# Optimization experiments

Hardware: AMD Instinct MI355X
Metric: run time of the kernel (lower is better)

Reference implementation:

```python
import jax, jax.numpy as jnp
import numpy as np

BN_EPS = 1e-5
K = 3  # kernel size


def conv2d(x, w, b, pad):
    y = jax.lax.conv_general_dilated(
        x, w, window_strides=(1, 1), padding=[(pad, pad), (pad, pad)],
        dimension_numbers=('NCHW', 'OIHW', 'NCHW'))
    return y + b[None, :, None, None]


def setup_inputs() -> dict:
    key = jax.random.key(0)
    ks = jax.random.split(key, 4)
    B, C, H, W, O = 8, 256, 64, 64, 256
    x = jax.random.normal(ks[0], (B, C, H, W), dtype=jnp.float32)
    # offset/mask conv: 3*dg*k*k = 27 out channels; small init -> small offsets
    w_off = jax.random.normal(ks[1], (27, C, K, K), dtype=jnp.float32) * 0.01
    b_off = jnp.zeros((27,), dtype=jnp.float32)
    # main deformable conv weight/bias
    w = jax.random.normal(ks[2], (O, C, K, K), dtype=jnp.float32) * 0.05
    b = jnp.zeros((O,), dtype=jnp.float32)
    # BatchNorm (inference) params / running stats
    gamma = jnp.ones((O,), dtype=jnp.float32)
    beta = jnp.zeros((O,), dtype=jnp.float32)
    run_mean = jnp.zeros((O,), dtype=jnp.float32)
    run_var = jnp.ones((O,), dtype=jnp.float32)
    return {"x": x, "w_off": w_off, "b_off": b_off, "w": w, "b": b,
            "gamma": gamma, "beta": beta, "run_mean": run_mean, "run_var": run_var}


def _dcn_bn_relu(x, w_off, b_off, w, b, gamma, beta, run_mean, run_var):
    B, C, H, W = x.shape
    KK = K * K
    # offset + modulation mask (DCNv2): channels [0:9]=dy, [9:18]=dx, [18:27]=mask
    om = conv2d(x, w_off, b_off, pad=1)            # [B, 27, H, W]
    dy, dx = om[:, :KK], om[:, KK:2 * KK]          # [B, 9, H, W]
    mod = jax.nn.sigmoid(om[:, 2 * KK:])           # [B, 9, H, W]

    ky, kx = jnp.meshgrid(jnp.arange(K), jnp.arange(K), indexing='ij')
    # base sampling grid: out pixel + dilation*(k - center), padding=1
    base_y = jnp.arange(H, dtype=jnp.float32)[None, :, None] - 1.0 + ky.reshape(KK, 1, 1)
    base_x = jnp.arange(W, dtype=jnp.float32)[None, None, :] - 1.0 + kx.reshape(KK, 1, 1)
    py = base_y[None] + dy                          # [B, 9, H, W]
    px = base_x[None] + dx

    y0 = jnp.floor(py); x0 = jnp.floor(px)
    fy = py - y0; fx = px - x0
    y0 = y0.astype(jnp.int32); x0 = x0.astype(jnp.int32)

    x_flat = x.reshape(B, C, H * W)
    gather = jax.vmap(lambda xf, idx: xf[:, idx])   # ([C,HW],[9,H,W]) -> [C,9,H,W]

    def corner(yi, xi, wgt):
        valid = (yi >= 0) & (yi < H) & (xi >= 0) & (xi < W)
        idx = jnp.clip(yi, 0, H - 1) * W + jnp.clip(xi, 0, W - 1)
        val = gather(x_flat, idx)                   # [B, C, 9, H, W]
        return val * (wgt * valid.astype(wgt.dtype))[:, None]

    sampled = (corner(y0,     x0,     (1 - fy) * (1 - fx))
               + corner(y0,     x0 + 1, (1 - fy) * fx)
               + corner(y0 + 1, x0,     fy * (1 - fx))
               + corner(y0 + 1, x0 + 1, fy * fx))    # [B, C, 9, H, W]
    sampled = sampled * mod[:, None]                 # modulation

    O = w.shape[0]
    out = jnp.einsum('bckhw,ock->bohw', sampled, w.reshape(O, C, KK))
    out = out + b[None, :, None, None]

    # BatchNorm2d (inference) + ReLU
    inv = gamma / jnp.sqrt(run_var + BN_EPS)
    out = out * inv[None, :, None, None] + (beta - run_mean * inv)[None, :, None, None]
    return jax.nn.relu(out)


def reference(x, w_off, b_off, w, b, gamma, beta, run_mean, run_var):
    return _dcn_bn_relu(x, w_off, b_off, w, b, gamma, beta, run_mean, run_var)
```

## Files before the change

### kernel.cpp

```cpp
#include <hip/hip_runtime.h>
#include <math.h>

#define B_   8
#define C_   256
#define H_   64
#define W_   64
#define O_   256
#define KK_  9
#define CK_  2304
#define HW_  4096
#define BN_EPS 1e-5f

typedef __bf16 bf16x8 __attribute__((ext_vector_type(8)));
typedef float  f32x4  __attribute__((ext_vector_type(4)));

static __device__ __forceinline__ unsigned short f2bf(float f) {
    unsigned int u = __float_as_uint(f);
    unsigned int r = (u + 0x7fffu + ((u >> 16) & 1u)) >> 16;
    return (unsigned short)r;
}
static __device__ __forceinline__ unsigned int packbf2(float lo, float hi) {
    unsigned int ul = __float_as_uint(lo) + 0x8000u;
    unsigned int uh = __float_as_uint(hi) + 0x8000u;
    return __builtin_amdgcn_perm(uh, ul, 0x07060302u);
}
static __device__ __forceinline__ float bflo(unsigned int u) {
    return __uint_as_float(u << 16);
}
static __device__ __forceinline__ float bfhi(unsigned int u) {
    return __uint_as_float(u & 0xffff0000u);
}

__global__ __launch_bounds__(256) void prep_kernel(
    const float* __restrict__ x, const float* __restrict__ w,
    const float* __restrict__ w_off,
    unsigned short* __restrict__ xT, unsigned short* __restrict__ wKf,
    unsigned short* __restrict__ wof)
{
    __shared__ float tile[64][65];
    __shared__ float wbuf[4608];

    const int blk = blockIdx.x;
    const int tid = threadIdx.x, lane = tid & 63, tg = tid >> 6;

    if (blk < 512) {
        const int b = blk & 7, h = blk >> 3;
        const int hwb = h * W_;
#pragma unroll
        for (int ct = 0; ct < 4; ++ct) {
            const int c0 = ct * 64;
#pragma unroll
            for (int r = 0; r < 16; ++r) {
                int c_l = tg + r * 4;
                tile[c_l][lane] = x[((size_t)(b * C_ + c0 + c_l)) * HW_ + hwb + lane];
            }
            __syncthreads();
#pragma unroll
            for (int it = 0; it < 4; ++it) {
                const int hw_l = tg * 16 + it * 4 + (lane >> 4);
                const int c_l4 = (lane & 15) * 4;
                float v0 = tile[c_l4 + 0][hw_l];
                float v1 = tile[c_l4 + 1][hw_l];
                float v2 = tile[c_l4 + 2][hw_l];
                float v3 = tile[c_l4 + 3][hw_l];
                uint2 pk;
                pk.x = packbf2(v0, v1);
                pk.y = packbf2(v2, v3);
                *(uint2*)&xT[((size_t)(b * HW_ + hwb + hw_l)) * C_ + c0 + c_l4] = pk;
            }
            __syncthreads();
        }
    } else if (blk < 640) {
        const int t2 = blk - 512;
        const int NT = t2 >> 3, cb = t2 & 7;
#pragma unroll
        for (int i = 0; i < 18; ++i) {
            int j = i * 256 + tid;
            int o_l = j / 288, rest = j - o_l * 288;
            wbuf[o_l * 288 + rest] = w[(size_t)(NT * 16 + o_l) * CK_ + cb * 288 + rest];
        }
        __syncthreads();
#pragma unroll
        for (int i = 0; i < 18; ++i) {
            int d = i * 256 + tid;
            int tap = d >> 9, r5 = d & 511;
            int ln = r5 >> 3, e = r5 & 7;
            int n16 = ln & 15, q = ln >> 4;
            float val = wbuf[n16 * 288 + (q * 8 + e) * 9 + tap];
            wKf[((size_t)(NT * 72 + tap * 8 + cb) * 64 + ln) * 8 + e] = f2bf(val);
        }
    } else {
        const int t2 = blk - 640;
        const int NT = t2 >> 3, cb = t2 & 7;
#pragma unroll
        for (int i = 0; i < 18; ++i) {
            int j = i * 256 + tid;
            int o_l = j / 288, rest = j - o_l * 288;
            int o = NT * 16 + o_l;
            wbuf[o_l * 288 + rest] =
                (o < 27) ? w_off[(size_t)o * CK_ + cb * 288 + rest] : 0.f;
        }
        __syncthreads();
#pragma unroll
        for (int i = 0; i < 18; ++i) {
            int d = i * 256 + tid;
            int tap = d >> 9, r5 = d & 511;
            int ln = r5 >> 3, e = r5 & 7;
            int n16 = ln & 15, q = ln >> 4;
            float val = wbuf[n16 * 288 + (q * 8 + e) * 9 + tap];
            wof[((size_t)(NT * 72 + tap * 8 + cb) * 64 + ln) * 8 + e] = f2bf(val);
        }
    }
}

__global__ __launch_bounds__(512, 4) void dcn_fused_kernel(
    const unsigned short* __restrict__ xT, const unsigned short* __restrict__ wKf,
    const unsigned short* __restrict__ wof, const float* __restrict__ b_off,
    const float* __restrict__ bias, const float* __restrict__ gamma,
    const float* __restrict__ beta, const float* __restrict__ rmean,
    const float* __restrict__ rvar, float* __restrict__ out)
{
    __shared__ __align__(16) unsigned char smem[74528];
    unsigned short* rowbuf = (unsigned short*)smem;
    float4*         wgtv   = (float4*)smem;
    int4*           idxv   = (int4*)(smem + 9216);
    typedef float OmbT[27][64];
    OmbT& omb = *(OmbT*)(smem + 34848);
    typedef unsigned short AbufT[8][4][64][8];
    AbufT& Abuf = *(AbufT*)(smem + 41760);

    const int blk = blockIdx.x;
    const int b = blk & 7, h = blk >> 3;
    const int tid = threadIdx.x, lane = tid & 63, wv = tid >> 6;
    const int m16 = lane & 15, q = lane >> 4;

    if (tid < 33) {
        *(uint4*)&rowbuf[tid * 8] = make_uint4(0u, 0u, 0u, 0u);
    } else if (tid >= 256 && tid < 289) {
        *(uint4*)&rowbuf[65 * 264 + (tid - 256) * 8] = make_uint4(0u, 0u, 0u, 0u);
    }

    const int mi_a = wv & 3, nj_a = wv >> 2;
    f32x4 oacc = {0.f, 0.f, 0.f, 0.f};
    const uint4* wof4 = (const uint4*)wof;

    for (int r = 0; r < 3; ++r) {
        const int hh = h - 1 + r;
        const bool vr = (hh >= 0) && (hh < H_);
        __syncthreads();
        if (vr) {
            const uint4* src = (const uint4*)&xT[((size_t)(b * HW_ + hh * W_)) * C_];
#pragma unroll
            for (int i = 0; i < 4; ++i) {
                const int idx8 = i * 512 + tid;
                uint4 v = src[idx8];
                const int px = idx8 >> 5, c8 = (idx8 & 31) * 8;
                *(uint4*)&rowbuf[(px + 1) * 264 + c8] = v;
            }
        }
        __syncthreads();
        if (vr) {
#pragma unroll
            for (int s = 0; s < 3; ++s) {
                const unsigned short* arow = &rowbuf[(mi_a * 16 + m16 + s) * 264 + q * 8];
#pragma unroll
                for (int cc = 0; cc < 8; ++cc) {
                    bf16x8 a = *(const bf16x8*)&arow[cc * 32];
                    uint4 braw = wof4[(size_t)(nj_a * 72 + (r * 3 + s) * 8 + cc) * 64 + lane];
                    oacc = __builtin_amdgcn_mfma_f32_16x16x32_bf16(
                        a, __builtin_bit_cast(bf16x8, braw), oacc, 0, 0, 0);
                }
            }
        }
    }
    {
        const int t = nj_a * 16 + m16;
        if (t < 27) {
            const float bo = b_off[t];
            float s0 = oacc[0] + bo, s1 = oacc[1] + bo,
                  s2 = oacc[2] + bo, s3 = oacc[3] + bo;
            if (t >= 18) {
                s0 = 1.f / (1.f + expf(-s0));
                s1 = 1.f / (1.f + expf(-s1));
                s2 = 1.f / (1.f + expf(-s2));
                s3 = 1.f / (1.f + expf(-s3));
            }
            float4 rr; rr.x = s0; rr.y = s1; rr.z = s2; rr.w = s3;
            *(float4*)&omb[t][mi_a * 16 + q * 4] = rr;
        }
    }
    __syncthreads();

    for (int i = tid; i < 576; i += 512) {
        int p = i / 9, t = i - p * 9;
        float dy = omb[t][p];
        float dx = omb[t + 9][p];
        float md = omb[t + 18][p];
        float py = (float)(h - 1 + t / 3) + dy;
        float px = (float)(p - 1 + t % 3) + dx;
        float y0f = floorf(py), x0f = floorf(px);
        int   y0 = (int)y0f,    x0 = (int)x0f;
        float fy = py - y0f,    fx = px - x0f;
        int y0c = min(max(y0,     0), H_ - 1), y1c = min(max(y0 + 1, 0), H_ - 1);
        int x0c = min(max(x0,     0), W_ - 1), x1c = min(max(x0 + 1, 0), W_ - 1);
        float vy0 = (y0     >= 0 && y0     < H_) ? 1.f : 0.f;
        float vy1 = (y0 + 1 >= 0 && y0 + 1 < H_) ? 1.f : 0.f;
        float vx0 = (x0     >= 0 && x0     < W_) ? 1.f : 0.f;
        float vx1 = (x0 + 1 >= 0 && x0 + 1 < W_) ? 1.f : 0.f;
        wgtv[i] = make_float4((1.f - fy) * (1.f - fx) * vy0 * vx0 * md,
                              (1.f - fy) * fx         * vy0 * vx1 * md,
                              fy         * (1.f - fx) * vy1 * vx0 * md,
                              fy         * fx         * vy1 * vx1 * md);
        const int rowb = (b * HW_) * (C_ * 2);
        idxv[i] = make_int4(rowb + (y0c * W_ + x0c) * (C_ * 2),
                            rowb + (y0c * W_ + x1c) * (C_ * 2),
                            rowb + (y1c * W_ + x0c) * (C_ * 2),
                            rowb + (y1c * W_ + x1c) * (C_ * 2));
    }
    __syncthreads();

    f32x4 acc[4][2];
#pragma unroll
    for (int mi = 0; mi < 4; ++mi)
#pragma unroll
        for (int nj = 0; nj < 2; ++nj)
#pragma unroll
            for (int r = 0; r < 4; ++r) acc[mi][nj][r] = 0.f;

    const uint4* wKf4 = (const uint4*)wKf;
    const char*  xTb  = (const char*)xT;

    const int s_cc = lane >> 3;
    const int s_q2 = (lane >> 1) & 3;
    const int s_j0 = (lane & 1) * 4;
    const int s_xr = (s_q2 << 1) ^ s_cc;
    const int s_mi = wv >> 1;
    const int s_pb = (wv & 1) * 8;
    const int loff = lane * 8;

    const int r_row = lane ^ ((lane >> 4) << 1);

    for (int tap = 0; tap < 9; ++tap) {
        uint2 pk[8];
#pragma unroll
        for (int pp = 0; pp < 8; ++pp) {
            const int p = wv * 8 + pp;
            const int4   iq = idxv[p * 9 + tap];
            const float4 wq = wgtv[p * 9 + tap];
            const uint2 k0 = *(const uint2*)(xTb + iq.x + loff);
            const uint2 k1 = *(const uint2*)(xTb + iq.y + loff);
            const uint2 k2 = *(const uint2*)(xTb + iq.z + loff);
            const uint2 k3 = *(const uint2*)(xTb + iq.w + loff);
            float g0 = wq.x*bflo(k0.x) + wq.y*bflo(k1.x) + wq.z*bflo(k2.x) + wq.w*bflo(k3.x);
            float g1 = wq.x*bfhi(k0.x) + wq.y*bfhi(k1.x) + wq.z*bfhi(k2.x) + wq.w*bfhi(k3.x);
            float g2 = wq.x*bflo(k0.y) + wq.y*bflo(k1.y) + wq.z*bflo(k2.y) + wq.w*bflo(k3.y);
            float g3 = wq.x*bfhi(k0.y) + wq.y*bfhi(k1.y) + wq.z*bfhi(k2.y) + wq.w*bfhi(k3.y);
            pk[pp].x = packbf2(g0, g1);
            pk[pp].y = packbf2(g2, g3);
        }

        __syncthreads();
#pragma unroll
        for (int pp = 0; pp < 8; ++pp) {
            const int P   = s_pb + pp;
            const int row = (P ^ s_xr) | (s_q2 << 4);
            *(uint2*)&Abuf[s_cc][s_mi][row][s_j0] = pk[pp];
        }
        __syncthreads();

#pragma unroll
        for (int cc = 0; cc < 8; ++cc) {
            const int KC = tap * 8 + cc;
            const int rr = r_row ^ cc;
            uint4 braw[2];
#pragma unroll
            for (int nj = 0; nj < 2; ++nj)
                braw[nj] = wKf4[(size_t)((wv * 2 + nj) * 72 + KC) * 64 + lane];
            bf16x8 a[4];
#pragma unroll
            for (int mi = 0; mi < 4; ++mi)
                a[mi] = *(const bf16x8*)&Abuf[cc][mi][rr][0];
#pragma unroll
            for (int nj = 0; nj < 2; ++nj) {
                bf16x8 bb = __builtin_bit_cast(bf16x8, braw[nj]);
#pragma unroll
                for (int mi = 0; mi < 4; ++mi)
                    acc[mi][nj] = __builtin_amdgcn_mfma_f32_16x16x32_bf16(
                        a[mi], bb, acc[mi][nj], 0, 0, 0);
            }
        }
    }

#pragma unroll
    for (int nj = 0; nj < 2; ++nj) {
        const int o = wv * 32 + nj * 16 + (lane & 15);
        const float inv = gamma[o] * rsqrtf(rvar[o] + BN_EPS);
        const float sh  = beta[o] + (bias[o] - rmean[o]) * inv;
        float* ob = out + ((size_t)(b * O_ + o)) * HW_ + h * W_;
#pragma unroll
        for (int mi = 0; mi < 4; ++mi) {
            f32x4 v = acc[mi][nj];
            float4 r;
            r.x = fmaxf(v[0] * inv + sh, 0.f);
            r.y = fmaxf(v[1] * inv + sh, 0.f);
            r.z = fmaxf(v[2] * inv + sh, 0.f);
            r.w = fmaxf(v[3] * inv + sh, 0.f);
            *(float4*)&ob[mi * 16 + (lane >> 4) * 4] = r;
        }
    }
}

extern "C" void kernel_launch(void* const* d_in, const int* in_sizes, int n_in,
                              void* d_out, int out_size, void* d_ws, size_t ws_size,
                              hipStream_t stream) {
    const float* x     = (const float*)d_in[0];
    const float* w_off = (const float*)d_in[1];
    const float* b_off = (const float*)d_in[2];
    const float* w     = (const float*)d_in[3];
    const float* bias  = (const float*)d_in[4];
    const float* gamma = (const float*)d_in[5];
    const float* beta  = (const float*)d_in[6];
    const float* rmean = (const float*)d_in[7];
    const float* rvar  = (const float*)d_in[8];
    float* out = (float*)d_out;

    unsigned short* xT  = (unsigned short*)d_ws;
    unsigned short* wKf = xT + 8388608;
    unsigned short* wof = wKf + 589824;

    prep_kernel<<<656, 256, 0, stream>>>(x, w, w_off, xT, wKf, wof);
    dcn_fused_kernel<<<512, 512, 0, stream>>>(
        xT, wKf, wof, b_off, bias, gamma, beta, rmean, rvar, out);
}
```

Before: 180.4 us.

## Double-buffer deformable sampling tile and overlap gathers with MFMA per tap

Turns the per-tap gather-then-MFMA loop into a software pipeline. The sampled A tile is now double-buffered in LDS, so the bilinear gathers for tap+1 are issued, and their weighted sums written to the other buffer, while the MFMAs for the current tap run. Each tap then needs one barrier instead of two. Corner indices are stored as 16-bit pixel offsets instead of precomputed byte offsets, and the offset-map buffer is aliased with the A buffers, which needs an extra barrier; LDS use grows and register pressure rises from the prefetched gathers and weights.

```diff
diff --git a/kernel.cpp b/kernel.cpp
--- a/kernel.cpp
+++ b/kernel.cpp
@@ -29,6 +29,16 @@
 }
 static __device__ __forceinline__ float bfhi(unsigned int u) {
     return __uint_as_float(u & 0xffff0000u);
+}
+static __device__ __forceinline__ uint2 wsum(const uint2 k[4], float4 wq) {
+    float g0 = wq.x*bflo(k[0].x) + wq.y*bflo(k[1].x) + wq.z*bflo(k[2].x) + wq.w*bflo(k[3].x);
+    float g1 = wq.x*bfhi(k[0].x) + wq.y*bfhi(k[1].x) + wq.z*bfhi(k[2].x) + wq.w*bfhi(k[3].x);
+    float g2 = wq.x*bflo(k[0].y) + wq.y*bflo(k[1].y) + wq.z*bflo(k[2].y) + wq.w*bflo(k[3].y);
+    float g3 = wq.x*bfhi(k[0].y) + wq.y*bfhi(k[1].y) + wq.z*bfhi(k[2].y) + wq.w*bfhi(k[3].y);
+    uint2 pk;
+    pk.x = packbf2(g0, g1);
+    pk.y = packbf2(g2, g3);
+    return pk;
 }
 
 __global__ __launch_bounds__(256) void prep_kernel(
@@ -120,14 +130,14 @@
     const float* __restrict__ beta, const float* __restrict__ rmean,
     const float* __restrict__ rvar, float* __restrict__ out)
 {
-    __shared__ __align__(16) unsigned char smem[74528];
+    __shared__ __align__(16) unsigned char smem[79360];
     unsigned short* rowbuf = (unsigned short*)smem;
-    float4*         wgtv   = (float4*)smem;
-    int4*           idxv   = (int4*)(smem + 9216);
+    float4*  wgtv = (float4*)smem;
+    ushort4* idxv = (ushort4*)(smem + 9216);
     typedef float OmbT[27][64];
-    OmbT& omb = *(OmbT*)(smem + 34848);
-    typedef unsigned short AbufT[8][4][64][8];
-    AbufT& Abuf = *(AbufT*)(smem + 41760);
+    OmbT& omb = *(OmbT*)(smem + 13824);
+    typedef unsigned short AbufT[2][8][4][64][8];
+    AbufT& Abuf = *(AbufT*)(smem + 13824);
 
     const int blk = blockIdx.x;
     const int b = blk & 7, h = blk >> 3;
@@ -173,6 +183,8 @@
             }
         }
     }
+    __syncthreads();
+
     {
         const int t = nj_a * 16 + m16;
         if (t < 27) {
@@ -211,11 +223,12 @@
                               (1.f - fy) * fx         * vy0 * vx1 * md,
                               fy         * (1.f - fx) * vy1 * vx0 * md,
                               fy         * fx         * vy1 * vx1 * md);
-        const int rowb = (b * HW_) * (C_ * 2);
-        idxv[i] = make_int4(rowb + (y0c * W_ + x0c) * (C_ * 2),
-                            rowb + (y0c * W_ + x1c) * (C_ * 2),
-                            rowb + (y1c * W_ + x0c) * (C_ * 2),
-                            rowb + (y1c * W_ + x1c) * (C_ * 2));
+        ushort4 uu;
+        uu.x = (unsigned short)(y0c * W_ + x0c);
+        uu.y = (unsigned short)(y0c * W_ + x1c);
+        uu.z = (unsigned short)(y1c * W_ + x0c);
+        uu.w = (unsigned short)(y1c * W_ + x1c);
+        idxv[i] = uu;
     }
     __syncthreads();
 
@@ -228,7 +241,7 @@
             for (int r = 0; r < 4; ++r) acc[mi][nj][r] = 0.f;
 
     const uint4* wKf4 = (const uint4*)wKf;
-    const char*  xTb  = (const char*)xT;
+    const char* xTbL = (const char*)xT + (size_t)(b * HW_) * (C_ * 2) + lane * 8;
 
     const int s_cc = lane >> 3;
     const int s_q2 = (lane >> 1) & 3;
@@ -236,59 +249,123 @@
     const int s_xr = (s_q2 << 1) ^ s_cc;
     const int s_mi = wv >> 1;
     const int s_pb = (wv & 1) * 8;
-    const int loff = lane * 8;
 
     const int r_row = lane ^ ((lane >> 4) << 1);
 
+#pragma unroll
+    for (int hf = 0; hf < 2; ++hf) {
+        uint2 kr[4][4];
+#pragma unroll
+        for (int pp = 0; pp < 4; ++pp) {
+            const ushort4 iq = idxv[(wv * 8 + hf * 4 + pp) * 9];
+            kr[pp][0] = *(const uint2*)(xTbL + ((int)iq.x << 9));
+            kr[pp][1] = *(const uint2*)(xTbL + ((int)iq.y << 9));
+            kr[pp][2] = *(const uint2*)(xTbL + ((int)iq.z << 9));
+            kr[pp][3] = *(const uint2*)(xTbL + ((int)iq.w << 9));
+        }
+#pragma unroll
+        for (int pp = 0; pp < 4; ++pp) {
+            const float4 wq = wgtv[(wv * 8 + hf * 4 + pp) * 9];
+            uint2 pk = wsum(kr[pp], wq);
+            const int row = ((s_pb + hf * 4 + pp) ^ s_xr) | (s_q2 << 4);
+            *(uint2*)&Abuf[0][s_cc][s_mi][row][s_j0] = pk;
+        }
+    }
+    __syncthreads();
+
+#pragma unroll 1
     for (int tap = 0; tap < 9; ++tap) {
-        uint2 pk[8];
-#pragma unroll
-        for (int pp = 0; pp < 8; ++pp) {
-            const int p = wv * 8 + pp;
-            const int4   iq = idxv[p * 9 + tap];
-            const float4 wq = wgtv[p * 9 + tap];
-            const uint2 k0 = *(const uint2*)(xTb + iq.x + loff);
-            const uint2 k1 = *(const uint2*)(xTb + iq.y + loff);
-            const uint2 k2 = *(const uint2*)(xTb + iq.z + loff);
-            const uint2 k3 = *(const uint2*)(xTb + iq.w + loff);
-            float g0 = wq.x*bflo(k0.x) + wq.y*bflo(k1.x) + wq.z*bflo(k2.x) + wq.w*bflo(k3.x);
-            float g1 = wq.x*bfhi(k0.x) + wq.y*bfhi(k1.x) + wq.z*bfhi(k2.x) + wq.w*bfhi(k3.x);
-            float g2 = wq.x*bflo(k0.y) + wq.y*bflo(k1.y) + wq.z*bflo(k2.y) + wq.w*bflo(k3.y);
-            float g3 = wq.x*bfhi(k0.y) + wq.y*bfhi(k1.y) + wq.z*bfhi(k2.y) + wq.w*bfhi(k3.y);
-            pk[pp].x = packbf2(g0, g1);
-            pk[pp].y = packbf2(g2, g3);
-        }
-
-        __syncthreads();
-#pragma unroll
-        for (int pp = 0; pp < 8; ++pp) {
-            const int P   = s_pb + pp;
-            const int row = (P ^ s_xr) | (s_q2 << 4);
-            *(uint2*)&Abuf[s_cc][s_mi][row][s_j0] = pk[pp];
-        }
-        __syncthreads();
-
-#pragma unroll
-        for (int cc = 0; cc < 8; ++cc) {
-            const int KC = tap * 8 + cc;
+        const int cbuf = tap & 1, nbuf = cbuf ^ 1;
+        const bool pf = (tap < 8);
+
+        uint4 br[8];
+#pragma unroll
+        for (int cc = 0; cc < 4; ++cc)
+#pragma unroll
+            for (int nj = 0; nj < 2; ++nj)
+                br[cc * 2 + nj] =
+                    wKf4[(size_t)((wv * 2 + nj) * 72 + tap * 8 + cc) * 64 + lane];
+        uint2 kr[4][4];
+        if (pf) {
+#pragma unroll
+            for (int pp = 0; pp < 4; ++pp) {
+                const ushort4 iq = idxv[(wv * 8 + pp) * 9 + tap + 1];
+                kr[pp][0] = *(const uint2*)(xTbL + ((int)iq.x << 9));
+                kr[pp][1] = *(const uint2*)(xTbL + ((int)iq.y << 9));
+                kr[pp][2] = *(const uint2*)(xTbL + ((int)iq.z << 9));
+                kr[pp][3] = *(const uint2*)(xTbL + ((int)iq.w << 9));
+            }
+        }
+#pragma unroll
+        for (int cc = 0; cc < 4; ++cc) {
             const int rr = r_row ^ cc;
-            uint4 braw[2];
-#pragma unroll
-            for (int nj = 0; nj < 2; ++nj)
-                braw[nj] = wKf4[(size_t)((wv * 2 + nj) * 72 + KC) * 64 + lane];
             bf16x8 a[4];
 #pragma unroll
             for (int mi = 0; mi < 4; ++mi)
-                a[mi] = *(const bf16x8*)&Abuf[cc][mi][rr][0];
+                a[mi] = *(const bf16x8*)&Abuf[cbuf][cc][mi][rr][0];
 #pragma unroll
             for (int nj = 0; nj < 2; ++nj) {
-                bf16x8 bb = __builtin_bit_cast(bf16x8, braw[nj]);
+                bf16x8 bb = __builtin_bit_cast(bf16x8, br[cc * 2 + nj]);
 #pragma unroll
                 for (int mi = 0; mi < 4; ++mi)
                     acc[mi][nj] = __builtin_amdgcn_mfma_f32_16x16x32_bf16(
                         a[mi], bb, acc[mi][nj], 0, 0, 0);
             }
         }
+        if (pf) {
+#pragma unroll
+            for (int pp = 0; pp < 4; ++pp) {
+                const float4 wq = wgtv[(wv * 8 + pp) * 9 + tap + 1];
+                uint2 pk = wsum(kr[pp], wq);
+                const int row = ((s_pb + pp) ^ s_xr) | (s_q2 << 4);
+                *(uint2*)&Abuf[nbuf][s_cc][s_mi][row][s_j0] = pk;
+            }
+        }
+
+        uint4 br2[8];
+#pragma unroll
+        for (int cc = 0; cc < 4; ++cc)
+#pragma unroll
+            for (int nj = 0; nj < 2; ++nj)
+                br2[cc * 2 + nj] =
+                    wKf4[(size_t)((wv * 2 + nj) * 72 + tap * 8 + cc + 4) * 64 + lane];
+        uint2 kr2[4][4];
+        if (pf) {
+#pragma unroll
+            for (int pp = 0; pp < 4; ++pp) {
+                const ushort4 iq = idxv[(wv * 8 + 4 + pp) * 9 + tap + 1];
+                kr2[pp][0] = *(const uint2*)(xTbL + ((int)iq.x << 9));
+                kr2[pp][1] = *(const uint2*)(xTbL + ((int)iq.y << 9));
+                kr2[pp][2] = *(const uint2*)(xTbL + ((int)iq.z << 9));
+                kr2[pp][3] = *(const uint2*)(xTbL + ((int)iq.w << 9));
+            }
+        }
+#pragma unroll
+        for (int cc = 0; cc < 4; ++cc) {
+            const int rr = r_row ^ (cc + 4);
+            bf16x8 a[4];
+#pragma unroll
+            for (int mi = 0; mi < 4; ++mi)
+                a[mi] = *(const bf16x8*)&Abuf[cbuf][cc + 4][mi][rr][0];
+#pragma unroll
+            for (int nj = 0; nj < 2; ++nj) {
+                bf16x8 bb = __builtin_bit_cast(bf16x8, br2[cc * 2 + nj]);
+#pragma unroll
+                for (int mi = 0; mi < 4; ++mi)
+                    acc[mi][nj] = __builtin_amdgcn_mfma_f32_16x16x32_bf16(
+                        a[mi], bb, acc[mi][nj], 0, 0, 0);
+            }
+        }
+        if (pf) {
+#pragma unroll
+            for (int pp = 0; pp < 4; ++pp) {
+                const float4 wq = wgtv[(wv * 8 + 4 + pp) * 9 + tap + 1];
+                uint2 pk = wsum(kr2[pp], wq);
+                const int row = ((s_pb + 4 + pp) ^ s_xr) | (s_q2 << 4);
+                *(uint2*)&Abuf[nbuf][s_cc][s_mi][row][s_j0] = pk;
+            }
+        }
+        __syncthreads();
     }
 
 #pragma unroll
```

New measurement: 279.2 us. 54.8% more time.

## Double-buffer weight fragment loads across MFMA pairs and raise wave priority

Applied to the files above, without the earlier changes.

Restructures the per-tap MFMA loop into four pairs of k-chunks, with B (weight) fragments prefetched into alternating register buffers one pair ahead and across tap boundaries. This hides global load latency behind the MFMA work. It also raises wave priority with s_setprio during the MFMA phase, stops unrolling the tap loop, and uses nontemporal stores for the output. The extra buffers raise register pressure, which could lower occupancy.

```diff
diff --git a/kernel.cpp b/kernel.cpp
--- a/kernel.cpp
+++ b/kernel.cpp
@@ -240,6 +240,38 @@
 
     const int r_row = lane ^ ((lane >> 4) << 1);
 
+    uint4 bA[4], bB[4];
+    auto loadB = [&](uint4* dst, int t_, int p_) {
+#pragma unroll
+        for (int c2 = 0; c2 < 2; ++c2)
+#pragma unroll
+            for (int nj = 0; nj < 2; ++nj)
+                dst[c2 * 2 + nj] =
+                    wKf4[(size_t)((wv * 2 + nj) * 72 + t_ * 8 + p_ * 2 + c2) * 64 + lane];
+    };
+    auto mfmaPair = [&](int p_, const uint4* Bf) {
+#pragma unroll
+        for (int c2 = 0; c2 < 2; ++c2) {
+            const int cc = p_ * 2 + c2;
+            const int rr = r_row ^ cc;
+            bf16x8 a[4];
+#pragma unroll
+            for (int mi = 0; mi < 4; ++mi)
+                a[mi] = *(const bf16x8*)&Abuf[cc][mi][rr][0];
+#pragma unroll
+            for (int nj = 0; nj < 2; ++nj) {
+                bf16x8 bb = __builtin_bit_cast(bf16x8, Bf[c2 * 2 + nj]);
+#pragma unroll
+                for (int mi = 0; mi < 4; ++mi)
+                    acc[mi][nj] = __builtin_amdgcn_mfma_f32_16x16x32_bf16(
+                        a[mi], bb, acc[mi][nj], 0, 0, 0);
+            }
+        }
+    };
+
+    loadB(bA, 0, 0);
+
+#pragma unroll 1
     for (int tap = 0; tap < 9; ++tap) {
         uint2 pk[8];
 #pragma unroll
@@ -268,27 +300,16 @@
         }
         __syncthreads();
 
-#pragma unroll
-        for (int cc = 0; cc < 8; ++cc) {
-            const int KC = tap * 8 + cc;
-            const int rr = r_row ^ cc;
-            uint4 braw[2];
-#pragma unroll
-            for (int nj = 0; nj < 2; ++nj)
-                braw[nj] = wKf4[(size_t)((wv * 2 + nj) * 72 + KC) * 64 + lane];
-            bf16x8 a[4];
-#pragma unroll
-            for (int mi = 0; mi < 4; ++mi)
-                a[mi] = *(const bf16x8*)&Abuf[cc][mi][rr][0];
-#pragma unroll
-            for (int nj = 0; nj < 2; ++nj) {
-                bf16x8 bb = __builtin_bit_cast(bf16x8, braw[nj]);
-#pragma unroll
-                for (int mi = 0; mi < 4; ++mi)
-                    acc[mi][nj] = __builtin_amdgcn_mfma_f32_16x16x32_bf16(
-                        a[mi], bb, acc[mi][nj], 0, 0, 0);
-            }
-        }
+        __builtin_amdgcn_s_setprio(1);
+        loadB(bB, tap, 1);
+        mfmaPair(0, bA);
+        loadB(bA, tap, 2);
+        mfmaPair(1, bB);
+        loadB(bB, tap, 3);
+        mfmaPair(2, bA);
+        if (tap < 8) loadB(bA, tap + 1, 0);
+        mfmaPair(3, bB);
+        __builtin_amdgcn_s_setprio(0);
     }
 
 #pragma unroll
@@ -300,12 +321,12 @@
 #pragma unroll
         for (int mi = 0; mi < 4; ++mi) {
             f32x4 v = acc[mi][nj];
-            float4 r;
-            r.x = fmaxf(v[0] * inv + sh, 0.f);
-            r.y = fmaxf(v[1] * inv + sh, 0.f);
-            r.z = fmaxf(v[2] * inv + sh, 0.f);
-            r.w = fmaxf(v[3] * inv + sh, 0.f);
-            *(float4*)&ob[mi * 16 + (lane >> 4) * 4] = r;
+            f32x4 r;
+            r[0] = fmaxf(v[0] * inv + sh, 0.f);
+            r[1] = fmaxf(v[1] * inv + sh, 0.f);
+            r[2] = fmaxf(v[2] * inv + sh, 0.f);
+            r[3] = fmaxf(v[3] * inv + sh, 0.f);
+            __builtin_nontemporal_store(r, (f32x4*)&ob[mi * 16 + (lane >> 4) * 4]);
         }
     }
 }
```

After: 174.2 us. 1.04x faster.
